# Optimization experiments

Measured on AMD Instinct MI355X. Metric: run time of the kernel, lower is better.

The kernel has to match this reference:

```python
import jax, jax.numpy as jnp
import numpy as np

B, S, H, DH = 2, 4096, 8, 64
D = H * DH  # 512

def setup_inputs() -> dict:
    key = jax.random.key(0)
    ks = jax.random.split(key, 9)
    sc = 1.0 / np.sqrt(D)
    return {
        "hidden_states": jax.random.normal(ks[0], (B, S, D), jnp.float32),
        "Wq": jax.random.normal(ks[1], (D, D), jnp.float32) * sc,
        "bq": jax.random.normal(ks[2], (D,), jnp.float32) * 0.02,
        "Wk": jax.random.normal(ks[3], (D, D), jnp.float32) * sc,
        "bk": jax.random.normal(ks[4], (D,), jnp.float32) * 0.02,
        "Wv": jax.random.normal(ks[5], (D, D), jnp.float32) * sc,
        "bv": jax.random.normal(ks[6], (D,), jnp.float32) * 0.02,
        "Wo": jax.random.normal(ks[7], (D, D), jnp.float32) * sc,
        "bo": jax.random.normal(ks[8], (D,), jnp.float32) * 0.02,
    }

def _split_heads(t):
    # (B, S, H*DH) -> (B, H, S, DH)
    b = t.shape[0]
    return t.reshape(b, S, H, DH).transpose(0, 2, 1, 3)

def reference(hidden_states, Wq, bq, Wk, bk, Wv, bv, Wo, bo):
    q = _split_heads(hidden_states @ Wq + bq)
    k = _split_heads(hidden_states @ Wk + bk)
    v = _split_heads(hidden_states @ Wv + bv)
    scale = 1.0 / jnp.sqrt(jnp.asarray(DH, q.dtype))
    energy = jnp.einsum('bhqd,bhkd->bhqk', q, k) * scale
    weights = jax.nn.softmax(energy, axis=-1)  # full O(S^2) matrix, as in source
    attended = jnp.einsum('bhqv,bhvd->bhqd', weights, v)
    merged = attended.transpose(0, 2, 1, 3).reshape(hidden_states.shape[0], S, D)
    return merged @ Wo + bo
```

## Files before the change

### kernel.cpp

```cpp
#include <hip/hip_runtime.h>
#include <cstdint>

typedef __bf16 bf16;
typedef __bf16 bf16x4 __attribute__((ext_vector_type(4)));
typedef __bf16 bf16x8 __attribute__((ext_vector_type(8)));
typedef float floatx4 __attribute__((ext_vector_type(4)));

#define MFMA32(a, b, c) __builtin_amdgcn_mfma_f32_16x16x32_bf16((a), (b), (c), 0, 0, 0)
#define MFMA16(a, b, c) __builtin_amdgcn_mfma_f32_16x16x16bf16_1k((a), (b), (c), 0, 0, 0)

__device__ inline bf16x8 cvt8(const float* p) {
    float4 u = *(const float4*)p;
    float4 v = *(const float4*)(p + 4);
    bf16x8 r;
    r[0] = (bf16)u.x; r[1] = (bf16)u.y; r[2] = (bf16)u.z; r[3] = (bf16)u.w;
    r[4] = (bf16)v.x; r[5] = (bf16)v.y; r[6] = (bf16)v.z; r[7] = (bf16)v.w;
    return r;
}

__global__ __launch_bounds__(256) void k_transpose(
    const float* __restrict__ w0, const float* __restrict__ w1,
    const float* __restrict__ w2, const float* __restrict__ w3,
    bf16* __restrict__ o0, bf16* __restrict__ o1,
    bf16* __restrict__ o2, bf16* __restrict__ o3)
{
    __shared__ float t[32][33];
    const float* in;
    bf16* out;
    switch (blockIdx.z) {
        case 0: in = w0; out = o0; break;
        case 1: in = w1; out = o1; break;
        case 2: in = w2; out = o2; break;
        default: in = w3; out = o3; break;
    }
    const int tx = threadIdx.x & 31;
    const int ty = threadIdx.x >> 5;
    const int r0 = blockIdx.y * 32;
    const int c0 = blockIdx.x * 32;
    #pragma unroll
    for (int i = 0; i < 32; i += 8)
        t[ty + i][tx] = in[(size_t)(r0 + ty + i) * 512 + c0 + tx];
    __syncthreads();
    #pragma unroll
    for (int i = 0; i < 32; i += 8)
        out[(size_t)(c0 + ty + i) * 512 + r0 + tx] = (bf16)t[tx][ty + i];
}

__global__ __launch_bounds__(256) void k_cvtx(
    const float* __restrict__ X, bf16* __restrict__ Xb)
{
    const size_t idx = ((size_t)blockIdx.x * 256 + threadIdx.x) * 8;
    *(bf16x8*)(Xb + idx) = cvt8(X + idx);
}

__global__ __launch_bounds__(256) void k_qkv(
    const bf16* __restrict__ Xb, const bf16* __restrict__ Wcat,
    const float* __restrict__ bq, const float* __restrict__ bk, const float* __restrict__ bv,
    bf16* __restrict__ Qs, bf16* __restrict__ Ks, bf16* __restrict__ Vt)
{
    __shared__ __align__(16) unsigned char smem[36864];
    uint4* Al = (uint4*)smem;
    uint4* Bl = (uint4*)(smem + 16384);

    const int tid  = threadIdx.x;
    const int w    = tid >> 6;
    const int lane = tid & 63;
    const int col  = lane & 15;
    const int quad = lane >> 4;
    const int m0 = blockIdx.x * 128;
    const int n0 = blockIdx.y * 128;

    const bf16* gA0 = Xb   + (size_t)(m0 + (tid >> 2)) * 512 + (tid & 3) * 8;
    const bf16* gA1 = gA0 + 64 * 512;
    const bf16* gB0 = Wcat + (size_t)(n0 + (tid >> 2)) * 512 + (tid & 3) * 8;
    const bf16* gB1 = gB0 + 64 * 512;

    const floatx4 zf = {0.f, 0.f, 0.f, 0.f};
    floatx4 acc[4][4];
    #pragma unroll
    for (int a = 0; a < 4; ++a)
        #pragma unroll
        for (int b = 0; b < 4; ++b) acc[a][b] = zf;

    Al[tid]       = *(const uint4*)gA0;
    Al[tid + 256] = *(const uint4*)gA1;
    Bl[tid]       = *(const uint4*)gB0;
    Bl[tid + 256] = *(const uint4*)gB1;
    __syncthreads();

    const int mb = (w & 1) * 64;
    const int nb = (w >> 1) * 64;

    int buf = 0;
    for (int kk = 0; kk < 16; ++kk) {
        const int kn = ((kk + 1) & 15) * 32;
        const uint4 pa0 = *(const uint4*)(gA0 + kn);
        const uint4 pa1 = *(const uint4*)(gA1 + kn);
        const uint4 pb0 = *(const uint4*)(gB0 + kn);
        const uint4 pb1 = *(const uint4*)(gB1 + kn);

        const uint4* A4 = Al + buf * 512;
        const uint4* B4 = Bl + buf * 512;
        bf16x8 af[4], bfr[4];
        #pragma unroll
        for (int t = 0; t < 4; ++t) {
            union { uint4 u; bf16x8 v; } ca, cb;
            ca.u = A4[(mb + 16 * t + col) * 4 + quad];
            cb.u = B4[(nb + 16 * t + col) * 4 + quad];
            af[t] = ca.v;
            bfr[t] = cb.v;
        }
        #pragma unroll
        for (int tm = 0; tm < 4; ++tm)
            #pragma unroll
            for (int tn = 0; tn < 4; ++tn)
                acc[tm][tn] = MFMA32(af[tm], bfr[tn], acc[tm][tn]);

        const int nbuf = buf ^ 1;
        Al[nbuf * 512 + tid]       = pa0;
        Al[nbuf * 512 + tid + 256] = pa1;
        Bl[nbuf * 512 + tid]       = pb0;
        Bl[nbuf * 512 + tid + 256] = pb1;
        __syncthreads();
        buf = nbuf;
    }

    bf16* ep = (bf16*)smem + (size_t)w * 64 * 72;

    const int which = blockIdx.y >> 2;
    const int nbase = (blockIdx.y & 3) * 128 + nb;
    const int h  = nbase >> 6;
    const int mw = m0 + mb;
    const int b  = mw >> 12;
    const int s0 = mw & 4095;
    const float qsc = 0.125f * 1.44269504088896f;

    if (which == 2) {
        #pragma unroll
        for (int tn = 0; tn < 4; ++tn) {
            const int d = 16 * tn + col;
            const float bb = bv[nbase + d];
            #pragma unroll
            for (int tm = 0; tm < 4; ++tm) {
                union { bf16 e[4]; uint2 u; } pk;
                #pragma unroll
                for (int r = 0; r < 4; ++r) pk.e[r] = (bf16)(acc[tm][tn][r] + bb);
                *(uint2*)(ep + d * 72 + 16 * tm + 4 * quad) = pk.u;
            }
        }
    } else {
        const float* bias = (which == 0) ? bq : bk;
        const float sc = (which == 0) ? qsc : 1.0f;
        #pragma unroll
        for (int tn = 0; tn < 4; ++tn) {
            const int d = 16 * tn + col;
            const float bb = bias[nbase + d];
            #pragma unroll
            for (int tm = 0; tm < 4; ++tm)
                #pragma unroll
                for (int r = 0; r < 4; ++r)
                    ep[(16 * tm + 4 * quad + r) * 72 + d] = (bf16)((acc[tm][tn][r] + bb) * sc);
        }
    }

    asm volatile("" ::: "memory");

    const int rl = lane >> 3;
    const int ch = lane & 7;
    bf16* gbase;
    size_t rowstride;
    if (which == 2) {
        gbase = Vt + (((size_t)b * 8 + h) * 64) * 4096 + s0;
        rowstride = 4096;
    } else {
        bf16* P = (which == 0) ? Qs : Ks;
        gbase = P + (((size_t)b * 8 + h) * 4096 + s0) * 64;
        rowstride = 64;
    }
    #pragma unroll
    for (int it = 0; it < 8; ++it) {
        const int row = it * 8 + rl;
        const uint4 v = *(const uint4*)(ep + row * 72 + ch * 8);
        *(uint4*)(gbase + (size_t)row * rowstride + ch * 8) = v;
    }
}

__global__ __launch_bounds__(256, 2) void k_attn(
    const bf16* __restrict__ Qs, const bf16* __restrict__ Ks, const bf16* __restrict__ Vt,
    bf16* __restrict__ att)
{
    __shared__ uint4 Klds[2][256];
    __shared__ uint4 Vlds[2][256];

    const int tid  = threadIdx.x;
    const int w    = tid >> 6;
    const int lane = tid & 63;
    const int col  = lane & 15;
    const int quad = lane >> 4;
    const int i    = blockIdx.x;
    const int bh   = ((i & 7) << 1) | ((i >> 3) & 1);
    const int q0   = (i >> 4) * 128 + w * 32;

    const bf16* Qb = Qs + (size_t)bh * 262144;
    const bf16* Kb = Ks + (size_t)bh * 262144;
    const bf16* Vb = Vt + (size_t)bh * 262144;

    const int rK  = tid >> 3;
    const int lcK = (tid & 7) ^ (rK & 7);
    const bf16* gK = Kb + (size_t)rK * 64 + lcK * 8;
    const int pV  = tid >> 3;
    const int ccV = (tid & 7) ^ (pV & 7);
    const int dV  = 2 * pV + (ccV >> 2);
    const int cV  = ccV & 3;
    const bf16* gV = Vb + (size_t)dV * 4096 + cV * 8;

    bf16x8 aq[2][2];
    #pragma unroll
    for (int s = 0; s < 2; ++s)
        #pragma unroll
        for (int c = 0; c < 2; ++c)
            aq[s][c] = *(const bf16x8*)(Qb + (size_t)(q0 + 16 * s + col) * 64 + 32 * c + quad * 8);

    const floatx4 zf = {0.f, 0.f, 0.f, 0.f};
    floatx4 o[2][4];
    float lsum[2] = {0.f, 0.f};
    #pragma unroll
    for (int s = 0; s < 2; ++s)
        #pragma unroll
        for (int dt = 0; dt < 4; ++dt) o[s][dt] = zf;

    const int c1 = col & 1, ch = col >> 1, qh = quad >> 1, ql = quad & 1;

    Klds[0][tid] = *(const uint4*)gK;
    Vlds[0][tid] = *(const uint4*)gV;
    __syncthreads();

    int buf = 0;
    for (int kt = 0; kt < 4096; kt += 32) {
        const int kn = (kt + 32) & 4095;
        const uint4 kreg = *(const uint4*)(gK + (size_t)kn * 64);
        const uint4 vreg = *(const uint4*)(gV + kn);

        const uint4* Kl = Klds[buf];
        const uint2* Vl = (const uint2*)Vlds[buf];

        bf16x8 kf[2][2];
        #pragma unroll
        for (int t = 0; t < 2; ++t)
            #pragma unroll
            for (int c = 0; c < 2; ++c) {
                union { uint4 u; bf16x8 v; } cv;
                cv.u = Kl[(16 * t + col) * 8 + ((quad + 4 * c) ^ (col & 7))];
                kf[t][c] = cv.v;
            }
        bf16x4 vfrag[4][2];
        #pragma unroll
        for (int dt = 0; dt < 4; ++dt)
            #pragma unroll
            for (int t = 0; t < 2; ++t) {
                const int slot = (dt * 8 + ch) * 8 + ((c1 * 4 + 2 * t + qh) ^ ch);
                union { uint2 u; bf16x4 v; } cv;
                cv.u = Vl[slot * 2 + ql];
                vfrag[dt][t] = cv.v;
            }

        #pragma unroll
        for (int s = 0; s < 2; ++s) {
            bf16x4 pw[2];
            #pragma unroll
            for (int t = 0; t < 2; ++t) {
                floatx4 sc = MFMA32(kf[t][1], aq[s][1], MFMA32(kf[t][0], aq[s][0], zf));
                const float p0 = __builtin_amdgcn_exp2f(sc[0]);
                const float p1 = __builtin_amdgcn_exp2f(sc[1]);
                const float p2 = __builtin_amdgcn_exp2f(sc[2]);
                const float p3 = __builtin_amdgcn_exp2f(sc[3]);
                lsum[s] += (p0 + p1) + (p2 + p3);
                union { bf16 e[4]; bf16x4 v; } pk;
                pk.e[0] = (bf16)p0; pk.e[1] = (bf16)p1;
                pk.e[2] = (bf16)p2; pk.e[3] = (bf16)p3;
                pw[t] = pk.v;
            }
            #pragma unroll
            for (int dt = 0; dt < 4; ++dt) {
                o[s][dt] = MFMA16(vfrag[dt][0], pw[0], o[s][dt]);
                o[s][dt] = MFMA16(vfrag[dt][1], pw[1], o[s][dt]);
            }
        }

        Klds[buf ^ 1][tid] = kreg;
        Vlds[buf ^ 1][tid] = vreg;
        __syncthreads();
        buf ^= 1;
    }

    float inv[2];
    #pragma unroll
    for (int s = 0; s < 2; ++s) {
        float v = lsum[s];
        v += __shfl_xor(v, 16, 64);
        v += __shfl_xor(v, 32, 64);
        inv[s] = 1.0f / v;
    }

    const int b = bh >> 3;
    const int h = bh & 7;
    #pragma unroll
    for (int s = 0; s < 2; ++s)
        #pragma unroll
        for (int dt = 0; dt < 4; ++dt) {
            union { bf16 e[4]; uint2 u; } pk;
            #pragma unroll
            for (int r = 0; r < 4; ++r) pk.e[r] = (bf16)(o[s][dt][r] * inv[s]);
            const size_t row = (size_t)b * 4096 + q0 + 16 * s + col;
            *(uint2*)(att + row * 512 + h * 64 + 16 * dt + 4 * quad) = pk.u;
        }
}

__global__ __launch_bounds__(256) void k_oproj(
    const bf16* __restrict__ att, const bf16* __restrict__ Wto,
    const float* __restrict__ bo, float* __restrict__ out)
{
    __shared__ uint4 Al[2][512];
    __shared__ uint4 Bl[2][512];

    const int tid  = threadIdx.x;
    const int w    = tid >> 6;
    const int lane = tid & 63;
    const int col  = lane & 15;
    const int quad = lane >> 4;
    const int m0 = blockIdx.x * 128;
    const int n0 = blockIdx.y * 128;

    const bf16* gA0 = att + (size_t)(m0 + (tid >> 2)) * 512 + (tid & 3) * 8;
    const bf16* gA1 = gA0 + 64 * 512;
    const bf16* gB0 = Wto + (size_t)(n0 + (tid >> 2)) * 512 + (tid & 3) * 8;
    const bf16* gB1 = gB0 + 64 * 512;

    const floatx4 zf = {0.f, 0.f, 0.f, 0.f};
    floatx4 acc[4][4];
    #pragma unroll
    for (int a = 0; a < 4; ++a)
        #pragma unroll
        for (int b = 0; b < 4; ++b) acc[a][b] = zf;

    Al[0][tid]       = *(const uint4*)gA0;
    Al[0][tid + 256] = *(const uint4*)gA1;
    Bl[0][tid]       = *(const uint4*)gB0;
    Bl[0][tid + 256] = *(const uint4*)gB1;
    __syncthreads();

    const int mb = (w & 1) * 64;
    const int nb = (w >> 1) * 64;

    int buf = 0;
    for (int kk = 0; kk < 16; ++kk) {
        const int kn = ((kk + 1) & 15) * 32;
        const uint4 pa0 = *(const uint4*)(gA0 + kn);
        const uint4 pa1 = *(const uint4*)(gA1 + kn);
        const uint4 pb0 = *(const uint4*)(gB0 + kn);
        const uint4 pb1 = *(const uint4*)(gB1 + kn);

        const uint4* A4 = Al[buf];
        const uint4* B4 = Bl[buf];
        bf16x8 af[4], bfr[4];
        #pragma unroll
        for (int t = 0; t < 4; ++t) {
            union { uint4 u; bf16x8 v; } ca, cb;
            ca.u = A4[(mb + 16 * t + col) * 4 + quad];
            cb.u = B4[(nb + 16 * t + col) * 4 + quad];
            af[t] = ca.v;
            bfr[t] = cb.v;
        }
        #pragma unroll
        for (int tm = 0; tm < 4; ++tm)
            #pragma unroll
            for (int tn = 0; tn < 4; ++tn)
                acc[tm][tn] = MFMA32(af[tm], bfr[tn], acc[tm][tn]);

        Al[buf ^ 1][tid]       = pa0;
        Al[buf ^ 1][tid + 256] = pa1;
        Bl[buf ^ 1][tid]       = pb0;
        Bl[buf ^ 1][tid + 256] = pb1;
        __syncthreads();
        buf ^= 1;
    }

    #pragma unroll
    for (int tn = 0; tn < 4; ++tn) {
        const int n = n0 + nb + 16 * tn + col;
        const float bb = bo[n];
        #pragma unroll
        for (int tm = 0; tm < 4; ++tm)
            #pragma unroll
            for (int r = 0; r < 4; ++r) {
                const int m = m0 + mb + 16 * tm + quad * 4 + r;
                out[(size_t)m * 512 + n] = acc[tm][tn][r] + bb;
            }
    }
}

extern "C" void kernel_launch(void* const* d_in, const int* in_sizes, int n_in,
                              void* d_out, int out_size, void* d_ws, size_t ws_size,
                              hipStream_t stream)
{
    const float* X  = (const float*)d_in[0];
    const float* Wq = (const float*)d_in[1];
    const float* bq = (const float*)d_in[2];
    const float* Wk = (const float*)d_in[3];
    const float* bk = (const float*)d_in[4];
    const float* Wv = (const float*)d_in[5];
    const float* bv = (const float*)d_in[6];
    const float* Wo = (const float*)d_in[7];
    const float* bo = (const float*)d_in[8];

    bf16* Wtq = (bf16*)d_ws;
    bf16* Wtk = Wtq + 512 * 512;
    bf16* Wtv = Wtk + 512 * 512;
    bf16* Wto = Wtv + 512 * 512;
    bf16* Qs  = Wto + 512 * 512;
    bf16* Ks  = Qs + (size_t)16 * 4096 * 64;
    bf16* Vt  = Ks + (size_t)16 * 4096 * 64;
    bf16* att = Vt + (size_t)16 * 4096 * 64;

    bf16* Xb  = (bf16*)d_out;

    k_transpose<<<dim3(16, 16, 4), 256, 0, stream>>>(Wq, Wk, Wv, Wo, Wtq, Wtk, Wtv, Wto);
    k_cvtx<<<2048, 256, 0, stream>>>(X, Xb);
    k_qkv<<<dim3(64, 12), 256, 0, stream>>>(Xb, Wtq, bq, bk, bv, Qs, Ks, Vt);
    k_attn<<<512, 256, 0, stream>>>(Qs, Ks, Vt, att);
    k_oproj<<<dim3(64, 4), 256, 0, stream>>>(att, Wto, bo, (float*)d_out);
}
```

Before: 205.6 us.

## Split attention key range across two wave groups and merge partials in LDS

Doubles the attention block to 512 threads, with two halves of four waves each processing a separate half of the key sequence for the same query rows. After the loop, the second half writes its unnormalized output accumulators and row sums to shared memory, and the first half adds them in and normalizes before storing. This raises wave count and latency hiding per CU at the same grid size, and each wave's serial loop is halved. The cost is an extra LDS reduction, a larger shared-memory footprint per block, and a tighter register budget from the launch bounds.

```diff
diff --git a/kernel.cpp b/kernel.cpp
--- a/kernel.cpp
+++ b/kernel.cpp
@@ -185,35 +185,44 @@
     }
 }
 
-__global__ __launch_bounds__(256, 2) void k_attn(
+__global__ __launch_bounds__(512, 4) void k_attn(
     const bf16* __restrict__ Qs, const bf16* __restrict__ Ks, const bf16* __restrict__ Vt,
     bf16* __restrict__ att)
 {
-    __shared__ uint4 Klds[2][256];
-    __shared__ uint4 Vlds[2][256];
+    __shared__ __align__(16) unsigned char smem[33280];
+    uint4* Klds = (uint4*)smem;
+    uint4* Vlds = (uint4*)(smem + 16384);
+    float* Of   = (float*)smem;
+    float* Ls   = (float*)(smem + 32768);
 
     const int tid  = threadIdx.x;
     const int w    = tid >> 6;
+    const int hf   = w >> 2;
+    const int wq   = w & 3;
     const int lane = tid & 63;
     const int col  = lane & 15;
     const int quad = lane >> 4;
     const int i    = blockIdx.x;
     const int bh   = ((i & 7) << 1) | ((i >> 3) & 1);
-    const int q0   = (i >> 4) * 128 + w * 32;
+    const int q0   = (i >> 4) * 128 + wq * 32;
 
     const bf16* Qb = Qs + (size_t)bh * 262144;
-    const bf16* Kb = Ks + (size_t)bh * 262144;
-    const bf16* Vb = Vt + (size_t)bh * 262144;
-
-    const int rK  = tid >> 3;
-    const int lcK = (tid & 7) ^ (rK & 7);
+    const bf16* Kb = Ks + (size_t)bh * 262144 + (size_t)hf * 2048 * 64;
+    const bf16* Vb = Vt + (size_t)bh * 262144 + (size_t)hf * 2048;
+
+    const int t8  = tid & 255;
+    const int rK  = t8 >> 3;
+    const int lcK = (t8 & 7) ^ (rK & 7);
     const bf16* gK = Kb + (size_t)rK * 64 + lcK * 8;
-    const int pV  = tid >> 3;
-    const int ccV = (tid & 7) ^ (pV & 7);
+    const int pV  = t8 >> 3;
+    const int ccV = (t8 & 7) ^ (pV & 7);
     const int dV  = 2 * pV + (ccV >> 2);
     const int cV  = ccV & 3;
     const bf16* gV = Vb + (size_t)dV * 4096 + cV * 8;
 
+    uint4* Kl2 = Klds + hf * 512;
+    uint4* Vl2 = Vlds + hf * 512;
+
     bf16x8 aq[2][2];
     #pragma unroll
     for (int s = 0; s < 2; ++s)
@@ -229,20 +238,20 @@
         #pragma unroll
         for (int dt = 0; dt < 4; ++dt) o[s][dt] = zf;
 
-    const int c1 = col & 1, ch = col >> 1, qh = quad >> 1, ql = quad & 1;
-
-    Klds[0][tid] = *(const uint4*)gK;
-    Vlds[0][tid] = *(const uint4*)gV;
+    const int c1 = col & 1, ch2 = col >> 1, qh = quad >> 1, ql = quad & 1;
+
+    Kl2[t8] = *(const uint4*)gK;
+    Vl2[t8] = *(const uint4*)gV;
     __syncthreads();
 
     int buf = 0;
-    for (int kt = 0; kt < 4096; kt += 32) {
-        const int kn = (kt + 32) & 4095;
+    for (int kt = 0; kt < 2048; kt += 32) {
+        const int kn = (kt + 32) & 2047;
         const uint4 kreg = *(const uint4*)(gK + (size_t)kn * 64);
         const uint4 vreg = *(const uint4*)(gV + kn);
 
-        const uint4* Kl = Klds[buf];
-        const uint2* Vl = (const uint2*)Vlds[buf];
+        const uint4* Kl = Kl2 + buf * 256;
+        const uint2* Vl = (const uint2*)(Vl2 + buf * 256);
 
         bf16x8 kf[2][2];
         #pragma unroll
@@ -258,7 +267,7 @@
         for (int dt = 0; dt < 4; ++dt)
             #pragma unroll
             for (int t = 0; t < 2; ++t) {
-                const int slot = (dt * 8 + ch) * 8 + ((c1 * 4 + 2 * t + qh) ^ ch);
+                const int slot = (dt * 8 + ch2) * 8 + ((c1 * 4 + 2 * t + qh) ^ ch2);
                 union { uint2 u; bf16x4 v; } cv;
                 cv.u = Vl[slot * 2 + ql];
                 vfrag[dt][t] = cv.v;
@@ -287,33 +296,57 @@
             }
         }
 
-        Klds[buf ^ 1][tid] = kreg;
-        Vlds[buf ^ 1][tid] = vreg;
+        Kl2[(buf ^ 1) * 256 + t8] = kreg;
+        Vl2[(buf ^ 1) * 256 + t8] = vreg;
         __syncthreads();
         buf ^= 1;
     }
 
-    float inv[2];
+    float lv[2];
     #pragma unroll
     for (int s = 0; s < 2; ++s) {
         float v = lsum[s];
         v += __shfl_xor(v, 16, 64);
         v += __shfl_xor(v, 32, 64);
-        inv[s] = 1.0f / v;
-    }
-
-    const int b = bh >> 3;
-    const int h = bh & 7;
-    #pragma unroll
-    for (int s = 0; s < 2; ++s)
-        #pragma unroll
-        for (int dt = 0; dt < 4; ++dt) {
-            union { bf16 e[4]; uint2 u; } pk;
-            #pragma unroll
-            for (int r = 0; r < 4; ++r) pk.e[r] = (bf16)(o[s][dt][r] * inv[s]);
-            const size_t row = (size_t)b * 4096 + q0 + 16 * s + col;
-            *(uint2*)(att + row * 512 + h * 64 + 16 * dt + 4 * quad) = pk.u;
-        }
+        lv[s] = v;
+    }
+
+    float* op = Of + ((size_t)(wq * 64 + lane)) * 32;
+    if (hf == 1) {
+        #pragma unroll
+        for (int s = 0; s < 2; ++s)
+            #pragma unroll
+            for (int dt = 0; dt < 4; ++dt) {
+                const int f = s * 4 + dt;
+                *(floatx4*)(op + ((f + lane) & 7) * 4) = o[s][dt];
+            }
+        if (quad == 0) {
+            Ls[(wq * 2 + 0) * 16 + col] = lv[0];
+            Ls[(wq * 2 + 1) * 16 + col] = lv[1];
+        }
+    }
+    __syncthreads();
+    if (hf == 0) {
+        float inv[2];
+        #pragma unroll
+        for (int s = 0; s < 2; ++s)
+            inv[s] = 1.0f / (lv[s] + Ls[(wq * 2 + s) * 16 + col]);
+        const int b  = bh >> 3;
+        const int hh = bh & 7;
+        #pragma unroll
+        for (int s = 0; s < 2; ++s)
+            #pragma unroll
+            for (int dt = 0; dt < 4; ++dt) {
+                const int f = s * 4 + dt;
+                const floatx4 po = *(const floatx4*)(op + ((f + lane) & 7) * 4);
+                union { bf16 e[4]; uint2 u; } pk;
+                #pragma unroll
+                for (int r = 0; r < 4; ++r)
+                    pk.e[r] = (bf16)((o[s][dt][r] + po[r]) * inv[s]);
+                const size_t row = (size_t)b * 4096 + q0 + 16 * s + col;
+                *(uint2*)(att + row * 512 + hh * 64 + 16 * dt + 4 * quad) = pk.u;
+            }
+    }
 }
 
 __global__ __launch_bounds__(256) void k_oproj(
@@ -427,6 +460,6 @@
     k_transpose<<<dim3(16, 16, 4), 256, 0, stream>>>(Wq, Wk, Wv, Wo, Wtq, Wtk, Wtv, Wto);
     k_cvtx<<<2048, 256, 0, stream>>>(X, Xb);
     k_qkv<<<dim3(64, 12), 256, 0, stream>>>(Xb, Wtq, bq, bk, bv, Qs, Ks, Vt);
-    k_attn<<<512, 256, 0, stream>>>(Qs, Ks, Vt, att);
+    k_attn<<<512, 512, 0, stream>>>(Qs, Ks, Vt, att);
     k_oproj<<<dim3(64, 4), 256, 0, stream>>>(att, Wto, bo, (float*)d_out);
 }
```

New measurement: 205.4 us. About the same (-0.1%).
